# Kernel optimization log

Hardware: AMD Instinct MI355X
Metric: run time of the kernel (lower is better)

## Reference

```python
import jax, jax.numpy as jnp
import numpy as np

E, H, DK, DV = 768, 12, 64, 64
S, B = 8, 1024


def setup_inputs() -> dict:
    key = jax.random.key(0)
    ks = jax.random.split(key, 12)
    std = 1.0 / np.sqrt(E)
    inp = {
        "Q": jax.random.normal(ks[0], (S, B, E), jnp.float32),
        "K": jax.random.normal(ks[1], (S, B, E), jnp.float32),
        "V": jax.random.normal(ks[2], (S, B, E), jnp.float32),
        # projection weights, torch Linear convention: y = x @ W.T + b
        "Wq": jax.random.normal(ks[3], (H * DK, E), jnp.float32) * std,
        "bq": jax.random.normal(ks[4], (H * DK,), jnp.float32) * std,
        "Wk": jax.random.normal(ks[5], (H * DK, E), jnp.float32) * std,
        "bk": jax.random.normal(ks[6], (H * DK,), jnp.float32) * std,
        "Wv": jax.random.normal(ks[7], (H * DV, E), jnp.float32) * std,
        "bv": jax.random.normal(ks[8], (H * DV,), jnp.float32) * std,
        "Wo": jax.random.normal(ks[9], (E, H * DV), jnp.float32) * std,
        "bo": jax.random.normal(ks[10], (E,), jnp.float32) * std,
        "ln_g": jnp.ones((E,), jnp.float32),
        "ln_b": jnp.zeros((E,), jnp.float32),
    }
    return inp


def _attention(Q, K, V, Wq, bq, Wk, bk, Wv, bv, Wo, bo, ln_g, ln_b):
    s, b, _ = Q.shape
    # linear projections, then view(S,B,H,d).transpose(1,2) -> [S,H,B,d]
    q = (Q @ Wq.T + bq).reshape(s, b, H, DK).transpose(0, 2, 1, 3)
    k = (K @ Wk.T + bk).reshape(s, b, H, DK).transpose(0, 2, 1, 3)
    v = (V @ Wv.T + bv).reshape(s, b, H, DV).transpose(0, 2, 1, 3)
    # scores over the batch (size-B) axis: [S,H,B,B]
    scores = jnp.einsum("shbd,shcd->shbc", q, k) / jnp.sqrt(
        jnp.asarray(DK, jnp.float32))
    attn = jax.nn.softmax(scores, axis=-1)
    context = jnp.einsum("shbc,shcd->shbd", attn, v)  # [S,H,B,DV]
    context = context.transpose(0, 2, 1, 3).reshape(s, b, H * DV)
    out = context @ Wo.T + bo
    x = out + Q  # residual
    mu = jnp.mean(x, axis=-1, keepdims=True)
    var = jnp.mean((x - mu) ** 2, axis=-1, keepdims=True)
    normed = (x - mu) * jax.lax.rsqrt(var + 1e-5) * ln_g + ln_b
    return normed, attn


def reference(Q, K, V, Wq, bq, Wk, bk, Wv, bv, Wo, bo, ln_g, ln_b):
    return _attention(Q, K, V, Wq, bq, Wk, bk, Wv, bv, Wo, bo, ln_g, ln_b)
```

## Files before the change

kernel.cpp:

```cpp
#include <hip/hip_runtime.h>
#include <hip/hip_bf16.h>
#include <math.h>

#define Sd 8
#define Bd 1024
#define Ed 768
#define Hd 12
#define Dd 64
#define SBd 8192

typedef short bf16x8 __attribute__((ext_vector_type(8)));
typedef unsigned short u16x8 __attribute__((ext_vector_type(8)));
typedef float f32x4 __attribute__((ext_vector_type(4)));

#define QSC 0.18033688011112043f

static __device__ __forceinline__ unsigned short f2bf(float f) {
  unsigned int u = __builtin_bit_cast(unsigned int, f);
  u += 0x7fffu + ((u >> 16) & 1u);
  return (unsigned short)(u >> 16);
}

__global__ __launch_bounds__(256) void qkv_kernel(
    const float* __restrict__ Qin, const float* __restrict__ Kin,
    const float* __restrict__ Vin,
    const float* __restrict__ Wq, const float* __restrict__ bq,
    const float* __restrict__ Wk, const float* __restrict__ bk,
    const float* __restrict__ Wv, const float* __restrict__ bv,
    unsigned short* __restrict__ qo, unsigned short* __restrict__ ko,
    unsigned short* __restrict__ vo) {
  __shared__ unsigned short As[64 * 72];
  __shared__ unsigned short Bs[64 * 72];
  const float* X;
  const float* W;
  const float* bias;
  switch (blockIdx.z) {
    case 0: X = Qin; W = Wq; bias = bq; break;
    case 1: X = Kin; W = Wk; bias = bk; break;
    default: X = Vin; W = Wv; bias = bv; break;
  }
  const bool vswap = (blockIdx.z == 2);
  const int i0 = blockIdx.x * 64;
  const int h = blockIdx.y;
  const int j0 = h * 64;
  const int t = threadIdx.x;
  const int w = t >> 6, l = t & 63, lr = l & 15, lg = l >> 4;
  const int srow = t >> 2, skg = (t & 3) << 4;

  const float* Abase = vswap ? W : X;
  const float* Bbase = vswap ? X : W;
  const int arow0 = vswap ? j0 : i0;
  const int brow0 = vswap ? i0 : j0;

  f32x4 acc[4] = {};

  for (int k0 = 0; k0 < Ed; k0 += 64) {
    const float* ap = Abase + (size_t)(arow0 + srow) * Ed + k0 + skg;
    const float* bp = Bbase + (size_t)(brow0 + srow) * Ed + k0 + skg;
    float4 x0 = *(const float4*)ap;
    float4 x1 = *(const float4*)(ap + 4);
    float4 x2 = *(const float4*)(ap + 8);
    float4 x3 = *(const float4*)(ap + 12);
    float4 w0 = *(const float4*)bp;
    float4 w1 = *(const float4*)(bp + 4);
    float4 w2 = *(const float4*)(bp + 8);
    float4 w3 = *(const float4*)(bp + 12);
    u16x8 pa0, pa1, pb0, pb1;
    pa0[0] = f2bf(x0.x); pa0[1] = f2bf(x0.y); pa0[2] = f2bf(x0.z); pa0[3] = f2bf(x0.w);
    pa0[4] = f2bf(x1.x); pa0[5] = f2bf(x1.y); pa0[6] = f2bf(x1.z); pa0[7] = f2bf(x1.w);
    pa1[0] = f2bf(x2.x); pa1[1] = f2bf(x2.y); pa1[2] = f2bf(x2.z); pa1[3] = f2bf(x2.w);
    pa1[4] = f2bf(x3.x); pa1[5] = f2bf(x3.y); pa1[6] = f2bf(x3.z); pa1[7] = f2bf(x3.w);
    pb0[0] = f2bf(w0.x); pb0[1] = f2bf(w0.y); pb0[2] = f2bf(w0.z); pb0[3] = f2bf(w0.w);
    pb0[4] = f2bf(w1.x); pb0[5] = f2bf(w1.y); pb0[6] = f2bf(w1.z); pb0[7] = f2bf(w1.w);
    pb1[0] = f2bf(w2.x); pb1[1] = f2bf(w2.y); pb1[2] = f2bf(w2.z); pb1[3] = f2bf(w2.w);
    pb1[4] = f2bf(w3.x); pb1[5] = f2bf(w3.y); pb1[6] = f2bf(w3.z); pb1[7] = f2bf(w3.w);
    __syncthreads();
    *(u16x8*)&As[srow * 72 + skg] = pa0;
    *(u16x8*)&As[srow * 72 + skg + 8] = pa1;
    *(u16x8*)&Bs[srow * 72 + skg] = pb0;
    *(u16x8*)&Bs[srow * 72 + skg + 8] = pb1;
    __syncthreads();
#pragma unroll
    for (int ks = 0; ks < 2; ++ks) {
      bf16x8 a = *(const bf16x8*)&As[(w * 16 + lr) * 72 + ks * 32 + lg * 8];
#pragma unroll
      for (int ct = 0; ct < 4; ++ct) {
        bf16x8 bb = *(const bf16x8*)&Bs[(ct * 16 + lr) * 72 + ks * 32 + lg * 8];
        acc[ct] = __builtin_amdgcn_mfma_f32_16x16x32_bf16(a, bb, acc[ct], 0, 0, 0);
      }
    }
  }

  if (!vswap) {
    unsigned short* out = (blockIdx.z == 0) ? qo : ko;
    const float sc = (blockIdx.z == 0) ? QSC : 1.0f;
#pragma unroll
    for (int ct = 0; ct < 4; ++ct) {
#pragma unroll
      for (int r = 0; r < 4; ++r) {
        int i = i0 + w * 16 + lg * 4 + r;
        int d = ct * 16 + lr;
        float v = (acc[ct][r] + bias[h * 64 + d]) * sc;
        int s = i >> 10, b = i & 1023;
        out[((((size_t)s * Hd + h) * Bd + b) << 6) + d] = f2bf(v);
      }
    }
  } else {
#pragma unroll
    for (int ct = 0; ct < 4; ++ct) {
#pragma unroll
      for (int r = 0; r < 4; ++r) {
        int d = w * 16 + lg * 4 + r;
        int gcol = i0 + ct * 16 + lr;
        float v = acc[ct][r] + bias[h * 64 + d];
        int s = gcol >> 10, b = gcol & 1023;
        vo[(((size_t)s * Hd + h) * 64 + d) * Bd + b] = f2bf(v);
      }
    }
  }
}

__global__ __launch_bounds__(256) void attn_kernel(
    const unsigned short* __restrict__ qb, const unsigned short* __restrict__ kb,
    const unsigned short* __restrict__ vt, float* __restrict__ attn_out,
    unsigned short* __restrict__ ctx_out) {
  __shared__ unsigned short Ks[64 * 72];
  __shared__ unsigned short Vs[64 * 72];
  __shared__ unsigned short Pb[4][16 * 72];
  const int sh = blockIdx.y;
  const int s = sh / Hd, h = sh % Hd;
  const int row0 = blockIdx.x * 64;
  const size_t base = (size_t)sh * Bd * 64;
  const int t = threadIdx.x;
  const int w = t >> 6, l = t & 63, lr = l & 15, lg = l >> 4;
  const int srow = t >> 2, skg = (t & 3) << 4;

  const int qrow = row0 + w * 16 + lr;
  const bf16x8 aq0 = *(const bf16x8*)(qb + base + (size_t)qrow * 64 + lg * 8);
  const bf16x8 aq1 = *(const bf16x8*)(qb + base + (size_t)qrow * 64 + 32 + lg * 8);

  float lsum[4] = {0.f, 0.f, 0.f, 0.f};

  {
    const unsigned short* kp = kb + base + (size_t)srow * 64 + skg;
    u16x8 k0 = *(const u16x8*)kp;
    u16x8 k1 = *(const u16x8*)(kp + 8);
    for (int ct = 0; ct < 16; ++ct) {
      __syncthreads();
      *(u16x8*)&Ks[srow * 72 + skg] = k0;
      *(u16x8*)&Ks[srow * 72 + skg + 8] = k1;
      __syncthreads();
      if (ct < 15) {
        const unsigned short* kn = kb + base + (size_t)((ct + 1) * 64 + srow) * 64 + skg;
        k0 = *(const u16x8*)kn;
        k1 = *(const u16x8*)(kn + 8);
      }
      f32x4 scv[4] = {};
#pragma unroll
      for (int ks = 0; ks < 2; ++ks) {
        bf16x8 a = ks ? aq1 : aq0;
#pragma unroll
        for (int c2 = 0; c2 < 4; ++c2) {
          bf16x8 bb = *(const bf16x8*)&Ks[(c2 * 16 + lr) * 72 + ks * 32 + lg * 8];
          scv[c2] = __builtin_amdgcn_mfma_f32_16x16x32_bf16(a, bb, scv[c2], 0, 0, 0);
        }
      }
#pragma unroll
      for (int c2 = 0; c2 < 4; ++c2)
#pragma unroll
        for (int r = 0; r < 4; ++r)
          lsum[r] += __builtin_amdgcn_exp2f(scv[c2][r]);
    }
  }
#pragma unroll
  for (int r = 0; r < 4; ++r) {
    float s1 = lsum[r];
    s1 += __shfl_xor(s1, 1, 16);
    s1 += __shfl_xor(s1, 2, 16);
    s1 += __shfl_xor(s1, 4, 16);
    s1 += __shfl_xor(s1, 8, 16);
    lsum[r] = 1.0f / s1;
  }

  f32x4 cacc[4] = {};
  const unsigned short* vbase = vt + (size_t)sh * 64 * Bd;
  u16x8 k0, k1, v0, v1;
  {
    const unsigned short* kp = kb + base + (size_t)srow * 64 + skg;
    k0 = *(const u16x8*)kp;
    k1 = *(const u16x8*)(kp + 8);
    const unsigned short* vp = vbase + (size_t)srow * Bd + skg;
    v0 = *(const u16x8*)vp;
    v1 = *(const u16x8*)(vp + 8);
  }
  for (int ct = 0; ct < 16; ++ct) {
    __syncthreads();
    *(u16x8*)&Ks[srow * 72 + skg] = k0;
    *(u16x8*)&Ks[srow * 72 + skg + 8] = k1;
    *(u16x8*)&Vs[srow * 72 + skg] = v0;
    *(u16x8*)&Vs[srow * 72 + skg + 8] = v1;
    __syncthreads();
    if (ct < 15) {
      const unsigned short* kn = kb + base + (size_t)((ct + 1) * 64 + srow) * 64 + skg;
      k0 = *(const u16x8*)kn;
      k1 = *(const u16x8*)(kn + 8);
      const unsigned short* vn = vbase + (size_t)srow * Bd + (ct + 1) * 64 + skg;
      v0 = *(const u16x8*)vn;
      v1 = *(const u16x8*)(vn + 8);
    }
    f32x4 scv[4] = {};
#pragma unroll
    for (int ks = 0; ks < 2; ++ks) {
      bf16x8 a = ks ? aq1 : aq0;
#pragma unroll
      for (int c2 = 0; c2 < 4; ++c2) {
        bf16x8 bb = *(const bf16x8*)&Ks[(c2 * 16 + lr) * 72 + ks * 32 + lg * 8];
        scv[c2] = __builtin_amdgcn_mfma_f32_16x16x32_bf16(a, bb, scv[c2], 0, 0, 0);
      }
    }
#pragma unroll
    for (int c2 = 0; c2 < 4; ++c2) {
#pragma unroll
      for (int r = 0; r < 4; ++r) {
        float p = __builtin_amdgcn_exp2f(scv[c2][r]) * lsum[r];
        int row = row0 + w * 16 + lg * 4 + r;
        __builtin_nontemporal_store(
            p, &attn_out[((size_t)sh * Bd + row) * Bd + ct * 64 + c2 * 16 + lr]);
        Pb[w][(lg * 4 + r) * 72 + c2 * 16 + lr] = f2bf(p);
      }
    }
#pragma unroll
    for (int ks2 = 0; ks2 < 2; ++ks2) {
      bf16x8 pa = *(const bf16x8*)&Pb[w][lr * 72 + ks2 * 32 + lg * 8];
#pragma unroll
      for (int dt = 0; dt < 4; ++dt) {
        bf16x8 bv = *(const bf16x8*)&Vs[(dt * 16 + lr) * 72 + ks2 * 32 + lg * 8];
        cacc[dt] = __builtin_amdgcn_mfma_f32_16x16x32_bf16(pa, bv, cacc[dt], 0, 0, 0);
      }
    }
  }

#pragma unroll
  for (int dt = 0; dt < 4; ++dt) {
#pragma unroll
    for (int r = 0; r < 4; ++r) {
      int row = row0 + w * 16 + lg * 4 + r;
      size_t i = (size_t)s * Bd + row;
      int j = h * 64 + dt * 16 + lr;
      ctx_out[i * Ed + j] = f2bf(cacc[dt][r]);
    }
  }
}

__global__ __launch_bounds__(256) void proj_kernel(
    const unsigned short* __restrict__ ctx, const float* __restrict__ Wo,
    const float* __restrict__ bo, const float* __restrict__ Qin,
    float* __restrict__ xout) {
  __shared__ unsigned short As[64 * 72];
  __shared__ unsigned short Bs[64 * 72];
  const int i0 = blockIdx.x * 64;
  const int j0 = blockIdx.y * 64;
  const int t = threadIdx.x;
  const int w = t >> 6, l = t & 63, lr = l & 15, lg = l >> 4;
  const int srow = t >> 2, skg = (t & 3) << 4;

  f32x4 acc[4] = {};

  for (int k0 = 0; k0 < Ed; k0 += 64) {
    const unsigned short* ap = ctx + (size_t)(i0 + srow) * Ed + k0 + skg;
    u16x8 a0 = *(const u16x8*)ap;
    u16x8 a1 = *(const u16x8*)(ap + 8);
    const float* wp = Wo + (size_t)(j0 + srow) * Ed + k0 + skg;
    float4 w0 = *(const float4*)wp;
    float4 w1 = *(const float4*)(wp + 4);
    float4 w2 = *(const float4*)(wp + 8);
    float4 w3 = *(const float4*)(wp + 12);
    u16x8 pb0, pb1;
    pb0[0] = f2bf(w0.x); pb0[1] = f2bf(w0.y); pb0[2] = f2bf(w0.z); pb0[3] = f2bf(w0.w);
    pb0[4] = f2bf(w1.x); pb0[5] = f2bf(w1.y); pb0[6] = f2bf(w1.z); pb0[7] = f2bf(w1.w);
    pb1[0] = f2bf(w2.x); pb1[1] = f2bf(w2.y); pb1[2] = f2bf(w2.z); pb1[3] = f2bf(w2.w);
    pb1[4] = f2bf(w3.x); pb1[5] = f2bf(w3.y); pb1[6] = f2bf(w3.z); pb1[7] = f2bf(w3.w);
    __syncthreads();
    *(u16x8*)&As[srow * 72 + skg] = a0;
    *(u16x8*)&As[srow * 72 + skg + 8] = a1;
    *(u16x8*)&Bs[srow * 72 + skg] = pb0;
    *(u16x8*)&Bs[srow * 72 + skg + 8] = pb1;
    __syncthreads();
#pragma unroll
    for (int ks = 0; ks < 2; ++ks) {
      bf16x8 a = *(const bf16x8*)&As[(w * 16 + lr) * 72 + ks * 32 + lg * 8];
#pragma unroll
      for (int ct = 0; ct < 4; ++ct) {
        bf16x8 bb = *(const bf16x8*)&Bs[(ct * 16 + lr) * 72 + ks * 32 + lg * 8];
        acc[ct] = __builtin_amdgcn_mfma_f32_16x16x32_bf16(a, bb, acc[ct], 0, 0, 0);
      }
    }
  }

#pragma unroll
  for (int ct = 0; ct < 4; ++ct) {
#pragma unroll
    for (int r = 0; r < 4; ++r) {
      int i = i0 + w * 16 + lg * 4 + r;
      int j = j0 + ct * 16 + lr;
      float v = acc[ct][r] + bo[j] + Qin[(size_t)i * Ed + j];
      xout[(size_t)i * Ed + j] = v;
    }
  }
}

__global__ __launch_bounds__(256) void ln_kernel(
    const float* __restrict__ x, const float* __restrict__ g,
    const float* __restrict__ bb, float* __restrict__ out) {
  const int i = blockIdx.x;
  const int t = threadIdx.x;
  const float* xr = x + (size_t)i * Ed;
  float v0 = xr[t], v1 = xr[t + 256], v2 = xr[t + 512];
  float s1 = v0 + v1 + v2;
  float s2 = v0 * v0 + v1 * v1 + v2 * v2;
#pragma unroll
  for (int mk = 1; mk < 64; mk <<= 1) {
    s1 += __shfl_xor(s1, mk, 64);
    s2 += __shfl_xor(s2, mk, 64);
  }
  __shared__ float red[8];
  const int w = t >> 6, l = t & 63;
  if (l == 0) { red[w] = s1; red[w + 4] = s2; }
  __syncthreads();
  s1 = red[0] + red[1] + red[2] + red[3];
  s2 = red[4] + red[5] + red[6] + red[7];
  float mu = s1 * (1.0f / 768.0f);
  float var = s2 * (1.0f / 768.0f) - mu * mu;
  float rs = rsqrtf(var + 1e-5f);
  float* orow = out + (size_t)i * Ed;
  orow[t] = (v0 - mu) * rs * g[t] + bb[t];
  orow[t + 256] = (v1 - mu) * rs * g[t + 256] + bb[t + 256];
  orow[t + 512] = (v2 - mu) * rs * g[t + 512] + bb[t + 512];
}

extern "C" void kernel_launch(void* const* d_in, const int* in_sizes, int n_in,
                              void* d_out, int out_size, void* d_ws, size_t ws_size,
                              hipStream_t stream) {
  (void)in_sizes; (void)n_in; (void)out_size; (void)ws_size;
  const float* Qin = (const float*)d_in[0];
  const float* Kin = (const float*)d_in[1];
  const float* Vin = (const float*)d_in[2];
  const float* Wq = (const float*)d_in[3];
  const float* bq = (const float*)d_in[4];
  const float* Wk = (const float*)d_in[5];
  const float* bk = (const float*)d_in[6];
  const float* Wv = (const float*)d_in[7];
  const float* bv = (const float*)d_in[8];
  const float* Wo = (const float*)d_in[9];
  const float* bo = (const float*)d_in[10];
  const float* ln_g = (const float*)d_in[11];
  const float* ln_b = (const float*)d_in[12];

  float* outp = (float*)d_out;
  float* normed = outp;
  float* attn_out = outp + (size_t)SBd * Ed;

  char* ws = (char*)d_ws;
  unsigned short* qws = (unsigned short*)ws;
  unsigned short* kws = qws + 6291456;
  unsigned short* vws = kws + 6291456;
  unsigned short* ctxws = vws + 6291456;
  float* xws = (float*)(ws + (size_t)4 * 12582912);

  dim3 blk(256);
  hipLaunchKernelGGL(qkv_kernel, dim3(128, 12, 3), blk, 0, stream,
                     Qin, Kin, Vin, Wq, bq, Wk, bk, Wv, bv, qws, kws, vws);
  hipLaunchKernelGGL(attn_kernel, dim3(16, 96), blk, 0, stream,
                     qws, kws, vws, attn_out, ctxws);
  hipLaunchKernelGGL(proj_kernel, dim3(128, 12), blk, 0, stream,
                     ctxws, Wo, bo, Qin, xws);
  hipLaunchKernelGGL(ln_kernel, dim3(8192), blk, 0, stream,
                     xws, ln_g, ln_b, normed);
}
```

Before: 311.8 us.

## Use 128x128 register-blocked tiles for QKV and output projection GEMMs

The QKV and output-projection GEMMs move from 64x64 tiles, where each wave computes a 16x64 strip, to 128x128 tiles where each wave computes a 64x64 sub-tile of 4x4 MFMA fragments. Loads are coalesced by flat thread index and fp32 is packed to bf16 two values at a time. The goal is more operand reuse per LDS fragment and less global traffic per FLOP. The V path drops its operand swap and writes a transposed layout with strided scalar stores. Attention barriers become an explicit lgkmcnt wait plus s_barrier, and the larger tiles raise register pressure and cut the grid to fewer blocks.

```diff
diff --git a/kernel.cpp b/kernel.cpp
--- a/kernel.cpp
+++ b/kernel.cpp
@@ -15,13 +15,24 @@
 
 #define QSC 0.18033688011112043f
 
+#define BARRIER()                                        \
+  do {                                                   \
+    asm volatile("s_waitcnt lgkmcnt(0)" ::: "memory");   \
+    __builtin_amdgcn_s_barrier();                        \
+    asm volatile("" ::: "memory");                       \
+  } while (0)
+
 static __device__ __forceinline__ unsigned short f2bf(float f) {
   unsigned int u = __builtin_bit_cast(unsigned int, f);
   u += 0x7fffu + ((u >> 16) & 1u);
   return (unsigned short)(u >> 16);
 }
 
-__global__ __launch_bounds__(256) void qkv_kernel(
+static __device__ __forceinline__ unsigned int pk2(float lo, float hi) {
+  return (unsigned int)f2bf(lo) | ((unsigned int)f2bf(hi) << 16);
+}
+
+__global__ __launch_bounds__(256, 2) void qkv_kernel(
     const float* __restrict__ Qin, const float* __restrict__ Kin,
     const float* __restrict__ Vin,
     const float* __restrict__ Wq, const float* __restrict__ bq,
@@ -29,8 +40,8 @@
     const float* __restrict__ Wv, const float* __restrict__ bv,
     unsigned short* __restrict__ qo, unsigned short* __restrict__ ko,
     unsigned short* __restrict__ vo) {
-  __shared__ unsigned short As[64 * 72];
-  __shared__ unsigned short Bs[64 * 72];
+  __shared__ unsigned short As[128 * 72];
+  __shared__ unsigned short Bs[128 * 72];
   const float* X;
   const float* W;
   const float* bias;
@@ -39,82 +50,88 @@
     case 1: X = Kin; W = Wk; bias = bk; break;
     default: X = Vin; W = Wv; bias = bv; break;
   }
-  const bool vswap = (blockIdx.z == 2);
-  const int i0 = blockIdx.x * 64;
-  const int h = blockIdx.y;
-  const int j0 = h * 64;
+  const int i0 = blockIdx.x * 128;
+  const int j0 = blockIdx.y * 128;
   const int t = threadIdx.x;
   const int w = t >> 6, l = t & 63, lr = l & 15, lg = l >> 4;
-  const int srow = t >> 2, skg = (t & 3) << 4;
-
-  const float* Abase = vswap ? W : X;
-  const float* Bbase = vswap ? X : W;
-  const int arow0 = vswap ? j0 : i0;
-  const int brow0 = vswap ? i0 : j0;
-
-  f32x4 acc[4] = {};
+  const int wr = w >> 1, wc = w & 1;
+
+  f32x4 acc[4][4] = {};
 
   for (int k0 = 0; k0 < Ed; k0 += 64) {
-    const float* ap = Abase + (size_t)(arow0 + srow) * Ed + k0 + skg;
-    const float* bp = Bbase + (size_t)(brow0 + srow) * Ed + k0 + skg;
-    float4 x0 = *(const float4*)ap;
-    float4 x1 = *(const float4*)(ap + 4);
-    float4 x2 = *(const float4*)(ap + 8);
-    float4 x3 = *(const float4*)(ap + 12);
-    float4 w0 = *(const float4*)bp;
-    float4 w1 = *(const float4*)(bp + 4);
-    float4 w2 = *(const float4*)(bp + 8);
-    float4 w3 = *(const float4*)(bp + 12);
-    u16x8 pa0, pa1, pb0, pb1;
-    pa0[0] = f2bf(x0.x); pa0[1] = f2bf(x0.y); pa0[2] = f2bf(x0.z); pa0[3] = f2bf(x0.w);
-    pa0[4] = f2bf(x1.x); pa0[5] = f2bf(x1.y); pa0[6] = f2bf(x1.z); pa0[7] = f2bf(x1.w);
-    pa1[0] = f2bf(x2.x); pa1[1] = f2bf(x2.y); pa1[2] = f2bf(x2.z); pa1[3] = f2bf(x2.w);
-    pa1[4] = f2bf(x3.x); pa1[5] = f2bf(x3.y); pa1[6] = f2bf(x3.z); pa1[7] = f2bf(x3.w);
-    pb0[0] = f2bf(w0.x); pb0[1] = f2bf(w0.y); pb0[2] = f2bf(w0.z); pb0[3] = f2bf(w0.w);
-    pb0[4] = f2bf(w1.x); pb0[5] = f2bf(w1.y); pb0[6] = f2bf(w1.z); pb0[7] = f2bf(w1.w);
-    pb1[0] = f2bf(w2.x); pb1[1] = f2bf(w2.y); pb1[2] = f2bf(w2.z); pb1[3] = f2bf(w2.w);
-    pb1[4] = f2bf(w3.x); pb1[5] = f2bf(w3.y); pb1[6] = f2bf(w3.z); pb1[7] = f2bf(w3.w);
+    uint2 pa[8], pb[8];
+#pragma unroll
+    for (int q = 0; q < 8; ++q) {
+      int flat = t + 256 * q;
+      int row = flat >> 4;
+      int c4 = (flat & 15) * 4;
+      float4 va = *(const float4*)(X + (size_t)(i0 + row) * Ed + k0 + c4);
+      float4 vb = *(const float4*)(W + (size_t)(j0 + row) * Ed + k0 + c4);
+      pa[q] = make_uint2(pk2(va.x, va.y), pk2(va.z, va.w));
+      pb[q] = make_uint2(pk2(vb.x, vb.y), pk2(vb.z, vb.w));
+    }
     __syncthreads();
-    *(u16x8*)&As[srow * 72 + skg] = pa0;
-    *(u16x8*)&As[srow * 72 + skg + 8] = pa1;
-    *(u16x8*)&Bs[srow * 72 + skg] = pb0;
-    *(u16x8*)&Bs[srow * 72 + skg + 8] = pb1;
+#pragma unroll
+    for (int q = 0; q < 8; ++q) {
+      int flat = t + 256 * q;
+      int row = flat >> 4;
+      int c4 = (flat & 15) * 4;
+      *(uint2*)&As[row * 72 + c4] = pa[q];
+      *(uint2*)&Bs[row * 72 + c4] = pb[q];
+    }
     __syncthreads();
 #pragma unroll
     for (int ks = 0; ks < 2; ++ks) {
-      bf16x8 a = *(const bf16x8*)&As[(w * 16 + lr) * 72 + ks * 32 + lg * 8];
-#pragma unroll
-      for (int ct = 0; ct < 4; ++ct) {
-        bf16x8 bb = *(const bf16x8*)&Bs[(ct * 16 + lr) * 72 + ks * 32 + lg * 8];
-        acc[ct] = __builtin_amdgcn_mfma_f32_16x16x32_bf16(a, bb, acc[ct], 0, 0, 0);
-      }
-    }
-  }
-
-  if (!vswap) {
-    unsigned short* out = (blockIdx.z == 0) ? qo : ko;
-    const float sc = (blockIdx.z == 0) ? QSC : 1.0f;
-#pragma unroll
-    for (int ct = 0; ct < 4; ++ct) {
-#pragma unroll
-      for (int r = 0; r < 4; ++r) {
-        int i = i0 + w * 16 + lg * 4 + r;
-        int d = ct * 16 + lr;
-        float v = (acc[ct][r] + bias[h * 64 + d]) * sc;
-        int s = i >> 10, b = i & 1023;
-        out[((((size_t)s * Hd + h) * Bd + b) << 6) + d] = f2bf(v);
+      bf16x8 af[4], bf[4];
+#pragma unroll
+      for (int fr = 0; fr < 4; ++fr)
+        af[fr] = *(const bf16x8*)&As[(wr * 64 + fr * 16 + lr) * 72 + ks * 32 + lg * 8];
+#pragma unroll
+      for (int fc = 0; fc < 4; ++fc)
+        bf[fc] = *(const bf16x8*)&Bs[(wc * 64 + fc * 16 + lr) * 72 + ks * 32 + lg * 8];
+#pragma unroll
+      for (int fr = 0; fr < 4; ++fr)
+#pragma unroll
+        for (int fc = 0; fc < 4; ++fc)
+          acc[fr][fc] = __builtin_amdgcn_mfma_f32_16x16x32_bf16(af[fr], bf[fc], acc[fr][fc], 0, 0, 0);
+    }
+  }
+
+  const int z = blockIdx.z;
+  if (z < 2) {
+    unsigned short* out = (z == 0) ? qo : ko;
+    const float sc = (z == 0) ? QSC : 1.0f;
+#pragma unroll
+    for (int fr = 0; fr < 4; ++fr) {
+#pragma unroll
+      for (int fc = 0; fc < 4; ++fc) {
+        int colg = j0 + wc * 64 + fc * 16 + lr;
+        int h = colg >> 6, d = colg & 63;
+        float bv_ = bias[colg];
+#pragma unroll
+        for (int r = 0; r < 4; ++r) {
+          int i = i0 + wr * 64 + fr * 16 + lg * 4 + r;
+          int s = i >> 10, b = i & 1023;
+          float v = (acc[fr][fc][r] + bv_) * sc;
+          out[((((size_t)s * Hd + h) * Bd + b) << 6) + d] = f2bf(v);
+        }
       }
     }
   } else {
 #pragma unroll
-    for (int ct = 0; ct < 4; ++ct) {
-#pragma unroll
-      for (int r = 0; r < 4; ++r) {
-        int d = w * 16 + lg * 4 + r;
-        int gcol = i0 + ct * 16 + lr;
-        float v = acc[ct][r] + bias[h * 64 + d];
-        int s = gcol >> 10, b = gcol & 1023;
-        vo[(((size_t)s * Hd + h) * 64 + d) * Bd + b] = f2bf(v);
+    for (int fr = 0; fr < 4; ++fr) {
+#pragma unroll
+      for (int fc = 0; fc < 4; ++fc) {
+        int colg = j0 + wc * 64 + fc * 16 + lr;
+        int h = colg >> 6, d = colg & 63;
+        float bv_ = bias[colg];
+#pragma unroll
+        for (int r = 0; r < 4; ++r) {
+          int i = i0 + wr * 64 + fr * 16 + lg * 4 + r;
+          int s = i >> 10, b = i & 1023;
+          float v = acc[fr][fc][r] + bv_;
+          vo[(((size_t)s * Hd + h) * 64 + d) * Bd + b] = f2bf(v);
+        }
       }
     }
   }
@@ -146,10 +163,10 @@
     u16x8 k0 = *(const u16x8*)kp;
     u16x8 k1 = *(const u16x8*)(kp + 8);
     for (int ct = 0; ct < 16; ++ct) {
-      __syncthreads();
+      BARRIER();
       *(u16x8*)&Ks[srow * 72 + skg] = k0;
       *(u16x8*)&Ks[srow * 72 + skg + 8] = k1;
-      __syncthreads();
+      BARRIER();
       if (ct < 15) {
         const unsigned short* kn = kb + base + (size_t)((ct + 1) * 64 + srow) * 64 + skg;
         k0 = *(const u16x8*)kn;
@@ -194,12 +211,12 @@
     v1 = *(const u16x8*)(vp + 8);
   }
   for (int ct = 0; ct < 16; ++ct) {
-    __syncthreads();
+    BARRIER();
     *(u16x8*)&Ks[srow * 72 + skg] = k0;
     *(u16x8*)&Ks[srow * 72 + skg + 8] = k1;
     *(u16x8*)&Vs[srow * 72 + skg] = v0;
     *(u16x8*)&Vs[srow * 72 + skg + 8] = v1;
-    __syncthreads();
+    BARRIER();
     if (ct < 15) {
       const unsigned short* kn = kb + base + (size_t)((ct + 1) * 64 + srow) * 64 + skg;
       k0 = *(const u16x8*)kn;
@@ -252,59 +269,83 @@
   }
 }
 
-__global__ __launch_bounds__(256) void proj_kernel(
+__global__ __launch_bounds__(256, 2) void proj_kernel(
     const unsigned short* __restrict__ ctx, const float* __restrict__ Wo,
     const float* __restrict__ bo, const float* __restrict__ Qin,
     float* __restrict__ xout) {
-  __shared__ unsigned short As[64 * 72];
-  __shared__ unsigned short Bs[64 * 72];
-  const int i0 = blockIdx.x * 64;
-  const int j0 = blockIdx.y * 64;
+  __shared__ unsigned short As[128 * 72];
+  __shared__ unsigned short Bs[128 * 72];
+  const int i0 = blockIdx.x * 128;
+  const int j0 = blockIdx.y * 128;
   const int t = threadIdx.x;
   const int w = t >> 6, l = t & 63, lr = l & 15, lg = l >> 4;
-  const int srow = t >> 2, skg = (t & 3) << 4;
-
-  f32x4 acc[4] = {};
+  const int wr = w >> 1, wc = w & 1;
+
+  f32x4 acc[4][4] = {};
 
   for (int k0 = 0; k0 < Ed; k0 += 64) {
-    const unsigned short* ap = ctx + (size_t)(i0 + srow) * Ed + k0 + skg;
-    u16x8 a0 = *(const u16x8*)ap;
-    u16x8 a1 = *(const u16x8*)(ap + 8);
-    const float* wp = Wo + (size_t)(j0 + srow) * Ed + k0 + skg;
-    float4 w0 = *(const float4*)wp;
-    float4 w1 = *(const float4*)(wp + 4);
-    float4 w2 = *(const float4*)(wp + 8);
-    float4 w3 = *(const float4*)(wp + 12);
-    u16x8 pb0, pb1;
-    pb0[0] = f2bf(w0.x); pb0[1] = f2bf(w0.y); pb0[2] = f2bf(w0.z); pb0[3] = f2bf(w0.w);
-    pb0[4] = f2bf(w1.x); pb0[5] = f2bf(w1.y); pb0[6] = f2bf(w1.z); pb0[7] = f2bf(w1.w);
-    pb1[0] = f2bf(w2.x); pb1[1] = f2bf(w2.y); pb1[2] = f2bf(w2.z); pb1[3] = f2bf(w2.w);
-    pb1[4] = f2bf(w3.x); pb1[5] = f2bf(w3.y); pb1[6] = f2bf(w3.z); pb1[7] = f2bf(w3.w);
+    u16x8 pa[4];
+    uint2 pb[8];
+#pragma unroll
+    for (int q = 0; q < 4; ++q) {
+      int flat = t + 256 * q;
+      int row = flat >> 3;
+      int c8 = (flat & 7) * 8;
+      pa[q] = *(const u16x8*)(ctx + (size_t)(i0 + row) * Ed + k0 + c8);
+    }
+#pragma unroll
+    for (int q = 0; q < 8; ++q) {
+      int flat = t + 256 * q;
+      int row = flat >> 4;
+      int c4 = (flat & 15) * 4;
+      float4 vb = *(const float4*)(Wo + (size_t)(j0 + row) * Ed + k0 + c4);
+      pb[q] = make_uint2(pk2(vb.x, vb.y), pk2(vb.z, vb.w));
+    }
     __syncthreads();
-    *(u16x8*)&As[srow * 72 + skg] = a0;
-    *(u16x8*)&As[srow * 72 + skg + 8] = a1;
-    *(u16x8*)&Bs[srow * 72 + skg] = pb0;
-    *(u16x8*)&Bs[srow * 72 + skg + 8] = pb1;
+#pragma unroll
+    for (int q = 0; q < 4; ++q) {
+      int flat = t + 256 * q;
+      int row = flat >> 3;
+      int c8 = (flat & 7) * 8;
+      *(u16x8*)&As[row * 72 + c8] = pa[q];
+    }
+#pragma unroll
+    for (int q = 0; q < 8; ++q) {
+      int flat = t + 256 * q;
+      int row = flat >> 4;
+      int c4 = (flat & 15) * 4;
+      *(uint2*)&Bs[row * 72 + c4] = pb[q];
+    }
     __syncthreads();
 #pragma unroll
     for (int ks = 0; ks < 2; ++ks) {
-      bf16x8 a = *(const bf16x8*)&As[(w * 16 + lr) * 72 + ks * 32 + lg * 8];
-#pragma unroll
-      for (int ct = 0; ct < 4; ++ct) {
-        bf16x8 bb = *(const bf16x8*)&Bs[(ct * 16 + lr) * 72 + ks * 32 + lg * 8];
-        acc[ct] = __builtin_amdgcn_mfma_f32_16x16x32_bf16(a, bb, acc[ct], 0, 0, 0);
-      }
-    }
-  }
-
-#pragma unroll
-  for (int ct = 0; ct < 4; ++ct) {
-#pragma unroll
-    for (int r = 0; r < 4; ++r) {
-      int i = i0 + w * 16 + lg * 4 + r;
-      int j = j0 + ct * 16 + lr;
-      float v = acc[ct][r] + bo[j] + Qin[(size_t)i * Ed + j];
-      xout[(size_t)i * Ed + j] = v;
+      bf16x8 af[4], bf[4];
+#pragma unroll
+      for (int fr = 0; fr < 4; ++fr)
+        af[fr] = *(const bf16x8*)&As[(wr * 64 + fr * 16 + lr) * 72 + ks * 32 + lg * 8];
+#pragma unroll
+      for (int fc = 0; fc < 4; ++fc)
+        bf[fc] = *(const bf16x8*)&Bs[(wc * 64 + fc * 16 + lr) * 72 + ks * 32 + lg * 8];
+#pragma unroll
+      for (int fr = 0; fr < 4; ++fr)
+#pragma unroll
+        for (int fc = 0; fc < 4; ++fc)
+          acc[fr][fc] = __builtin_amdgcn_mfma_f32_16x16x32_bf16(af[fr], bf[fc], acc[fr][fc], 0, 0, 0);
+    }
+  }
+
+#pragma unroll
+  for (int fr = 0; fr < 4; ++fr) {
+#pragma unroll
+    for (int fc = 0; fc < 4; ++fc) {
+      int j = j0 + wc * 64 + fc * 16 + lr;
+      float bv_ = bo[j];
+#pragma unroll
+      for (int r = 0; r < 4; ++r) {
+        int i = i0 + wr * 64 + fr * 16 + lg * 4 + r;
+        float v = acc[fr][fc][r] + bv_ + Qin[(size_t)i * Ed + j];
+        xout[(size_t)i * Ed + j] = v;
+      }
     }
   }
 }
@@ -368,11 +409,11 @@
   float* xws = (float*)(ws + (size_t)4 * 12582912);
 
   dim3 blk(256);
-  hipLaunchKernelGGL(qkv_kernel, dim3(128, 12, 3), blk, 0, stream,
+  hipLaunchKernelGGL(qkv_kernel, dim3(64, 6, 3), blk, 0, stream,
                      Qin, Kin, Vin, Wq, bq, Wk, bk, Wv, bv, qws, kws, vws);
   hipLaunchKernelGGL(attn_kernel, dim3(16, 96), blk, 0, stream,
                      qws, kws, vws, attn_out, ctxws);
-  hipLaunchKernelGGL(proj_kernel, dim3(128, 12), blk, 0, stream,
+  hipLaunchKernelGGL(proj_kernel, dim3(64, 6), blk, 0, stream,
                      ctxws, Wo, bo, Qin, xws);
   hipLaunchKernelGGL(ln_kernel, dim3(8192), blk, 0, stream,
                      xws, ln_g, ln_b, normed);
```

After: 290.5 us. -6.8%, faster.
